# Performance work log

Hardware: AMD Instinct MI355X
Metric: run time of the kernel (lower is better)

The kernel has to match this reference:

```python
import jax, jax.numpy as jnp
import numpy as np


def _conv1x1(x, W, b):
    # x: (B,C,H,W), W: (O,C), b: (O,)
    return jnp.einsum('bchw,oc->bohw', x, W) + b[None, :, None, None]


def _maxpool2(x):
    B, C, H, W = x.shape
    return x.reshape(B, C, H // 2, 2, W // 2, 2).max(axis=(3, 5))


def setup_inputs() -> dict:
    key = jax.random.key(0)
    ks = jax.random.split(key, 6)
    B, C, H, W = 8, 1024, 64, 64
    DI, DO = 512, 1024
    std = 0.01  # matches nn.init.normal_(std=0.01)
    return {
        'x': jax.random.normal(ks[0], (B, C, H, W), dtype=jnp.float32),
        'W_theta': std * jax.random.normal(ks[1], (DI, C), dtype=jnp.float32),
        'b_theta': jnp.zeros((DI,), jnp.float32),
        'W_phi': std * jax.random.normal(ks[2], (DI, C), dtype=jnp.float32),
        'b_phi': jnp.zeros((DI,), jnp.float32),
        'W_g': std * jax.random.normal(ks[3], (DI, C), dtype=jnp.float32),
        'b_g': jnp.zeros((DI,), jnp.float32),
        'W_out': std * jax.random.normal(ks[4], (DO, DI), dtype=jnp.float32),
        'b_out': jnp.zeros((DO,), jnp.float32),
    }


def reference(x, W_theta, b_theta, W_phi, b_phi, W_g, b_g, W_out, b_out):
    B, C, H, W = x.shape
    di = W_theta.shape[0]
    scale = di ** (-0.5)
    # queries from full-res map: (B, di, N) with N = H*W
    theta = _conv1x1(x, W_theta, b_theta).reshape(B, di, H * W)
    # keys/values from 2x2-maxpooled map: (B, di, M), M = (H/2)*(W/2)
    px = _maxpool2(x)
    phi = _conv1x1(px, W_phi, b_phi).reshape(B, di, -1)
    g = _conv1x1(px, W_g, b_g).reshape(B, di, -1)
    # attention: (B, N, M)
    logits = jnp.einsum('bdn,bdm->bnm', theta, phi) * scale
    p = jax.nn.softmax(logits, axis=-1)
    # aggregate values: (B, di, N) -> (B, di, H, W)
    t = jnp.einsum('bdm,bnm->bdn', g, p).reshape(B, di, H, W)
    y = _conv1x1(t, W_out, b_out)
    return y + x
```

## Files before the change

### kernel.cpp

```cpp
#include <hip/hip_runtime.h>
#include <hip/hip_bf16.h>
#include <stdint.h>

typedef __bf16 bf16;
typedef __bf16 bf16x8 __attribute__((ext_vector_type(8)));
typedef __bf16 bf16x4 __attribute__((ext_vector_type(4)));
typedef float f32x4 __attribute__((ext_vector_type(4)));

#define GLOAD_LDS16(gptr, lptr)                                                        \
  __builtin_amdgcn_global_load_lds((const __attribute__((address_space(1))) void*)(gptr), \
                                   (__attribute__((address_space(3))) void*)(lptr), 16, 0, 0)

__global__ __launch_bounds__(256) void cast_f2b(const float* __restrict__ in,
                                                bf16* __restrict__ out, int n) {
  int i = (blockIdx.x * 256 + threadIdx.x) * 4;
  if (i >= n) return;
  const float4 v = *(const float4*)(in + i);
  bf16x4 o;
  o[0] = (bf16)v.x; o[1] = (bf16)v.y; o[2] = (bf16)v.z; o[3] = (bf16)v.w;
  *(bf16x4*)(out + i) = o;
}

__global__ __launch_bounds__(256) void zero_k(float* __restrict__ p, int n) {
  int i = blockIdx.x * 256 + threadIdx.x;
  if (i < n) p[i] = 0.f;
}

__global__ __launch_bounds__(256) void prep_kernel(const float* __restrict__ x,
                                                   bf16* __restrict__ xbT,
                                                   bf16* __restrict__ pxT) {
  const int b = blockIdx.y;
  x   += (size_t)b * 1024 * 4096;
  xbT += (size_t)b * 4096 * 1024;
  pxT += (size_t)b * 1024 * 1024;
  const int bid = blockIdx.x;
  const int h0 = bid & 31, ct = bid >> 5;
  const int tid = threadIdx.x;
  __shared__ float tile[64][129];
  const float* xs = x + (size_t)(ct * 64) * 4096 + h0 * 128;
#pragma unroll
  for (int e = 0; e < 8; ++e) {
    const int idx = e * 256 + tid;
    const int c = idx >> 5, n4 = (idx & 31) * 4;
    *(float4*)&tile[c][n4] = *(const float4*)&xs[(size_t)c * 4096 + n4];
  }
  __syncthreads();
  bf16* xo = xbT + (size_t)(h0 * 128) * 1024 + ct * 64;
#pragma unroll
  for (int e = 0; e < 4; ++e) {
    const int flat = e * 256 + tid;
    const int n = flat >> 3, c8 = (flat & 7) * 8;
    bf16x8 o;
#pragma unroll
    for (int j = 0; j < 8; ++j) o[j] = (bf16)tile[c8 + j][n];
    *(bf16x8*)&xo[(size_t)n * 1024 + c8] = o;
  }
  bf16* po = pxT + (size_t)(h0 * 32) * 1024 + ct * 64;
  {
    const int m = tid >> 3, c8 = (tid & 7) * 8;
    bf16x8 o;
#pragma unroll
    for (int j = 0; j < 8; ++j) {
      const int c = c8 + j;
      float v = fmaxf(fmaxf(tile[c][2 * m], tile[c][2 * m + 1]),
                      fmaxf(tile[c][64 + 2 * m], tile[c][64 + 2 * m + 1]));
      o[j] = (bf16)v;
    }
    *(bf16x8*)&po[(size_t)m * 1024 + c8] = o;
  }
}

template <int EPI>
__global__ __launch_bounds__(512, 4) void gemm256(
    const bf16* __restrict__ A, long long sA, int lda,
    const bf16* __restrict__ B, long long sB, int ldb,
    void* __restrict__ Cv, long long sC, int ldc, int K,
    const float* __restrict__ bias,
    const float* __restrict__ resid, long long sResid, float scale,
    float* __restrict__ rs_out) {
  const int z = blockIdx.z;
  A += (size_t)z * sA;
  B += (size_t)z * sB;
  const int tid = threadIdx.x;
  const int w = tid >> 6, lane = tid & 63;
  const int r16 = lane & 15, q4 = lane >> 4;
  const int wm = w >> 2, wn = w & 3;
  const long long tileM = (long long)blockIdx.x * 128;
  const long long tileN = (long long)blockIdx.y * 256;

  __shared__ bf16 As[2][4096];
  __shared__ bf16 Bs[2][8192];

  f32x4 acc[4][4] = {};

  const int srow = tid >> 2;
  const int skb  = (tid & 3) ^ ((srow >> 1) & 3);
  const char* Ag = (const char*)A + ((size_t)(tileM + srow) * lda + skb * 8) * 2;
  const char* Bg = (const char*)B + ((size_t)(tileN + srow) * ldb + skb * 8) * 2;
  const size_t b128 = (size_t)128 * ldb * 2;

  auto stage = [&](int T) {
    const int sl = T & 1;
    GLOAD_LDS16(Ag + (size_t)T * 64, &As[sl][w * 512]);
    GLOAD_LDS16(Bg + (size_t)T * 64, &Bs[sl][w * 512]);
    GLOAD_LDS16(Bg + (size_t)T * 64 + b128, &Bs[sl][4096 + w * 512]);
  };

  stage(0);
  const int NT = K >> 5;

  for (int T = 0; T < NT; ++T) {
    asm volatile("s_waitcnt vmcnt(0)" ::: "memory");
    __builtin_amdgcn_s_barrier();
    asm volatile("" ::: "memory");
    if (T + 1 < NT) stage(T + 1);
    const char* Asl = (const char*)&As[T & 1][0];
    const char* Bsl = (const char*)&Bs[T & 1][0];
    bf16x8 af[4], bf_[4];
#pragma unroll
    for (int mi = 0; mi < 4; ++mi) {
      const int row = wm * 64 + mi * 16 + r16;
      af[mi] = *(const bf16x8*)(Asl + row * 64 + ((q4 ^ ((row >> 1) & 3)) << 4));
    }
#pragma unroll
    for (int ni = 0; ni < 4; ++ni) {
      const int row = wn * 64 + ni * 16 + r16;
      bf_[ni] = *(const bf16x8*)(Bsl + row * 64 + ((q4 ^ ((row >> 1) & 3)) << 4));
    }
    __builtin_amdgcn_s_setprio(1);
#pragma unroll
    for (int mi = 0; mi < 4; ++mi)
#pragma unroll
      for (int ni = 0; ni < 4; ++ni)
        acc[mi][ni] = __builtin_amdgcn_mfma_f32_16x16x32_bf16(af[mi], bf_[ni], acc[mi][ni], 0, 0, 0);
    __builtin_amdgcn_s_setprio(0);
  }

  if constexpr (EPI == 4) {
    float* C = (float*)Cv + (size_t)z * sC;
    const float* rz = resid + (size_t)z * sResid;
#pragma unroll
    for (int a = 0; a < 4; ++a) {
      const int row0 = (int)tileM + wm * 64 + a * 16 + q4 * 4;
#pragma unroll
      for (int ni = 0; ni < 4; ++ni) {
        const int col = (int)tileN + wn * 64 + ni * 16 + r16;
#pragma unroll
        for (int r = 0; r < 4; ++r)
          C[(size_t)(row0 + r) * ldc + col] =
              acc[a][ni][r] + bias[row0 + r] + rz[(size_t)(row0 + r) * ldc + col];
      }
    }
  } else if constexpr (EPI == 5) {
    bf16* C = (bf16*)Cv + (size_t)z * sC;
    float* rsp = rs_out + (size_t)z * 4096;
#pragma unroll
    for (int a = 0; a < 4; ++a) {
      const int row0 = (int)tileM + wm * 64 + a * 16 + q4 * 4;
      float psum[4] = {0.f, 0.f, 0.f, 0.f};
#pragma unroll
      for (int ni = 0; ni < 4; ++ni) {
        const int col = (int)tileN + wn * 64 + ni * 16 + r16;
#pragma unroll
        for (int r = 0; r < 4; ++r) {
          float e = __expf(acc[a][ni][r]);
          psum[r] += e;
          C[(size_t)(row0 + r) * ldc + col] = (bf16)e;
        }
      }
#pragma unroll
      for (int r = 0; r < 4; ++r) {
        float v = psum[r];
        v += __shfl_xor(v, 1);
        v += __shfl_xor(v, 2);
        v += __shfl_xor(v, 4);
        v += __shfl_xor(v, 8);
        if (r16 == 0) atomicAdd(&rsp[row0 + r], v);
      }
    }
  } else if constexpr (EPI == 7) {
    bf16* C = (bf16*)Cv + (size_t)z * sC;
    const float* rsp = bias + (size_t)z * 4096;
#pragma unroll
    for (int a = 0; a < 4; ++a) {
      const int row0 = (int)tileM + wm * 64 + a * 16 + q4 * 4;
      float inv[4];
#pragma unroll
      for (int r = 0; r < 4; ++r) inv[r] = 1.0f / rsp[row0 + r];
#pragma unroll
      for (int ni = 0; ni < 4; ++ni) {
        const int col = (int)tileN + wn * 64 + ni * 16 + r16;
#pragma unroll
        for (int r = 0; r < 4; ++r)
          C[(size_t)(row0 + r) * ldc + col] = (bf16)(acc[a][ni][r] * inv[r]);
      }
    }
  } else if constexpr (EPI == 2) {
    bf16* C = (bf16*)Cv + (size_t)z * sC;
#pragma unroll
    for (int a = 0; a < 4; ++a) {
      const int row0 = (int)tileM + wm * 64 + a * 16 + q4 * 4;
#pragma unroll
      for (int ni = 0; ni < 4; ++ni) {
        const int col = (int)tileN + wn * 64 + ni * 16 + r16;
#pragma unroll
        for (int r = 0; r < 4; ++r)
          C[(size_t)(row0 + r) * ldc + col] = (bf16)(acc[a][ni][r] + bias[row0 + r]);
      }
    }
  } else {
    bf16* C = (bf16*)Cv + (size_t)z * sC;
#pragma unroll
    for (int a = 0; a < 4; ++a) {
      const int row0 = (int)tileM + wm * 64 + a * 16 + q4 * 4;
#pragma unroll
      for (int ni = 0; ni < 4; ++ni) {
        const int col = (int)tileN + wn * 64 + ni * 16 + r16;
        const float badd = bias[col];
#pragma unroll
        for (int r = 0; r < 4; ++r)
          C[(size_t)(row0 + r) * ldc + col] = (bf16)((acc[a][ni][r] + badd) * scale);
      }
    }
  }
}

extern "C" void kernel_launch(void* const* d_in, const int* in_sizes, int n_in,
                              void* d_out, int out_size, void* d_ws, size_t ws_size,
                              hipStream_t stream) {
  const float* x  = (const float*)d_in[0];
  const float* Wt = (const float*)d_in[1];
  const float* bt = (const float*)d_in[2];
  const float* Wp = (const float*)d_in[3];
  const float* bp = (const float*)d_in[4];
  const float* Wg = (const float*)d_in[5];
  const float* bg = (const float*)d_in[6];
  const float* Wo = (const float*)d_in[7];
  const float* bo = (const float*)d_in[8];
  float* out = (float*)d_out;

  const size_t MB = 1024ull * 1024ull;
  char* ws = (char*)d_ws;
  bf16* WtB = (bf16*)(ws + 0 * MB);
  bf16* WpB = (bf16*)(ws + 1 * MB);
  bf16* WgB = (bf16*)(ws + 2 * MB);
  bf16* WoB = (bf16*)(ws + 3 * MB);

  cast_f2b<<<512, 256, 0, stream>>>(Wt, WtB, 512 * 1024);
  cast_f2b<<<512, 256, 0, stream>>>(Wp, WpB, 512 * 1024);
  cast_f2b<<<512, 256, 0, stream>>>(Wg, WgB, 512 * 1024);
  cast_f2b<<<512, 256, 0, stream>>>(Wo, WoB, 1024 * 512);

  const float SCALE = 0.044194173824159216f;

  auto run_g6 = [&](int nb, int b0, bf16* tT) {
    gemm256<4><<<dim3(8, 16, nb), 512, 0, stream>>>(WoB, 0, 512, tT, 4096ll * 512, 512,
                                                    out + (size_t)b0 * 1024 * 4096,
                                                    1024ll * 4096, 4096, 512,
                                                    bo, x + (size_t)b0 * 1024 * 4096,
                                                    1024ll * 4096, 1.f, nullptr);
  };

  if (ws_size >= 164 * MB) {
    bf16* pxT    = (bf16*)(ws + 4 * MB);
    bf16* phiT   = (bf16*)(ws + 20 * MB);
    bf16* g      = (bf16*)(ws + 28 * MB);
    bf16* thetaT = (bf16*)(ws + 36 * MB);
    bf16* tT     = (bf16*)(ws + 68 * MB);
    bf16* xbT    = (bf16*)(ws + 100 * MB);
    bf16*  Pt   = (bf16*)d_out;
    float* rsum = (float*)((char*)d_out + 80 * MB);

    prep_kernel<<<dim3(512, 8), 256, 0, stream>>>(x, xbT, pxT);
    gemm256<1><<<dim3(32, 2, 8), 512, 0, stream>>>(xbT, 4096ll * 1024, 1024, WtB, 0, 1024,
                                                   thetaT, 4096ll * 512, 512, 1024,
                                                   bt, nullptr, 0, SCALE, nullptr);
    gemm256<1><<<dim3(8, 2, 8), 512, 0, stream>>>(pxT, 1024ll * 1024, 1024, WpB, 0, 1024,
                                                  phiT, 1024ll * 512, 512, 1024,
                                                  bp, nullptr, 0, 1.f, nullptr);
    gemm256<2><<<dim3(4, 4, 8), 512, 0, stream>>>(WgB, 0, 1024, pxT, 1024ll * 1024, 1024,
                                                  g, 512ll * 1024, 1024, 1024,
                                                  bg, nullptr, 0, 1.f, nullptr);
    zero_k<<<128, 256, 0, stream>>>(rsum, 32768);
    gemm256<5><<<dim3(32, 4, 8), 512, 0, stream>>>(thetaT, 4096ll * 512, 512,
                                                   phiT, 1024ll * 512, 512,
                                                   Pt, 4096ll * 1024, 1024, 512,
                                                   nullptr, nullptr, 0, 1.f, rsum);
    gemm256<7><<<dim3(32, 2, 8), 512, 0, stream>>>(Pt, 4096ll * 1024, 1024,
                                                   g, 512ll * 1024, 1024,
                                                   tT, 4096ll * 512, 512, 1024,
                                                   rsum, nullptr, 0, 1.f, nullptr);
    run_g6(8, 0, tT);
  } else if (ws_size >= 108 * MB) {
    bf16* pxT    = (bf16*)(ws + 4 * MB);
    bf16* phiT   = (bf16*)(ws + 20 * MB);
    bf16* g      = (bf16*)(ws + 28 * MB);
    bf16* thetaT = (bf16*)(ws + 36 * MB);
    bf16* tT     = (bf16*)(ws + 68 * MB);
    bf16* xbT    = (bf16*)(ws + 100 * MB);
    float* rsum = (float*)((char*)d_out + 80 * MB);
    for (int b = 0; b < 8; ++b) {
      prep_kernel<<<dim3(512, 1), 256, 0, stream>>>(x + (size_t)b * 1024 * 4096, xbT,
                                                    pxT + (size_t)b * 1024 * 1024);
      gemm256<1><<<dim3(32, 2, 1), 512, 0, stream>>>(xbT, 0, 1024, WtB, 0, 1024,
                                                     thetaT + (size_t)b * 4096 * 512, 0, 512,
                                                     1024, bt, nullptr, 0, SCALE, nullptr);
    }
    gemm256<1><<<dim3(8, 2, 8), 512, 0, stream>>>(pxT, 1024ll * 1024, 1024, WpB, 0, 1024,
                                                  phiT, 1024ll * 512, 512, 1024,
                                                  bp, nullptr, 0, 1.f, nullptr);
    gemm256<2><<<dim3(4, 4, 8), 512, 0, stream>>>(WgB, 0, 1024, pxT, 1024ll * 1024, 1024,
                                                  g, 512ll * 1024, 1024, 1024,
                                                  bg, nullptr, 0, 1.f, nullptr);
    for (int b = 0; b < 8; ++b) {
      bf16* Ptb = (bf16*)d_out + (size_t)b * 4096 * 1024;
      zero_k<<<16, 256, 0, stream>>>(rsum + (size_t)b * 4096, 4096);
      gemm256<5><<<dim3(32, 4, 1), 512, 0, stream>>>(thetaT + (size_t)b * 4096 * 512, 0, 512,
                                                     phiT + (size_t)b * 1024 * 512, 0, 512,
                                                     Ptb, 0, 1024, 512,
                                                     nullptr, nullptr, 0, 1.f,
                                                     rsum + (size_t)b * 4096);
      gemm256<7><<<dim3(32, 2, 1), 512, 0, stream>>>(Ptb, 0, 1024,
                                                     g + (size_t)b * 512 * 1024, 0, 1024,
                                                     tT + (size_t)b * 4096 * 512, 0, 512, 1024,
                                                     rsum + (size_t)b * 4096, nullptr, 0, 1.f,
                                                     nullptr);
    }
    run_g6(8, 0, tT);
  } else {
    float* rsum  = (float*)(ws + 4 * MB);
    bf16* pxT    = (bf16*)(ws + 5 * MB);
    bf16* phiT   = (bf16*)(ws + 7 * MB);
    bf16* g      = (bf16*)(ws + 8 * MB);
    bf16* thetaT = (bf16*)(ws + 9 * MB);
    bf16* tT     = (bf16*)(ws + 13 * MB);
    bf16* Pt     = (bf16*)(ws + 17 * MB);
    bf16* xbT    = (bf16*)(ws + 25 * MB);
    for (int b = 0; b < 8; ++b) {
      prep_kernel<<<dim3(512, 1), 256, 0, stream>>>(x + (size_t)b * 1024 * 4096, xbT, pxT);
      gemm256<1><<<dim3(32, 2, 1), 512, 0, stream>>>(xbT, 0, 1024, WtB, 0, 1024,
                                                     thetaT, 0, 512, 1024,
                                                     bt, nullptr, 0, SCALE, nullptr);
      gemm256<1><<<dim3(8, 2, 1), 512, 0, stream>>>(pxT, 0, 1024, WpB, 0, 1024,
                                                    phiT, 0, 512, 1024,
                                                    bp, nullptr, 0, 1.f, nullptr);
      gemm256<2><<<dim3(4, 4, 1), 512, 0, stream>>>(WgB, 0, 1024, pxT, 0, 1024,
                                                    g, 0, 1024, 1024,
                                                    bg, nullptr, 0, 1.f, nullptr);
      zero_k<<<16, 256, 0, stream>>>(rsum, 4096);
      gemm256<5><<<dim3(32, 4, 1), 512, 0, stream>>>(thetaT, 0, 512, phiT, 0, 512,
                                                     Pt, 0, 1024, 512,
                                                     nullptr, nullptr, 0, 1.f, rsum);
      gemm256<7><<<dim3(32, 2, 1), 512, 0, stream>>>(Pt, 0, 1024, g, 0, 1024,
                                                     tT, 0, 512, 1024,
                                                     rsum, nullptr, 0, 1.f, nullptr);
      run_g6(1, b, tT);
    }
  }
}
```

Measured before the change: 323.4 us.

## Reassociate output projection with values and fuse phi/g projections

Precomputes W2 = W_out·g per batch so the final GEMM multiplies W2 by the unnormalized attention matrix directly, dropping the separate P·g GEMM and the tT intermediate. The softmax normalization, bias and residual are applied in a new epilogue. The phi and g projections are merged into one GEMM with concatenated weights and biases. In exchange, the final GEMM's reduction length doubles, and a new W2 GEMM is added.

```diff
diff --git a/kernel.cpp b/kernel.cpp
--- a/kernel.cpp
+++ b/kernel.cpp
@@ -24,6 +24,14 @@
 __global__ __launch_bounds__(256) void zero_k(float* __restrict__ p, int n) {
   int i = blockIdx.x * 256 + threadIdx.x;
   if (i < n) p[i] = 0.f;
+}
+
+__global__ __launch_bounds__(256) void concat512(const float* __restrict__ a,
+                                                 const float* __restrict__ b,
+                                                 float* __restrict__ o) {
+  int i = blockIdx.x * 256 + threadIdx.x;
+  if (i < 512) o[i] = a[i];
+  else if (i < 1024) o[i] = b[i - 512];
 }
 
 __global__ __launch_bounds__(256) void prep_kernel(const float* __restrict__ x,
@@ -114,6 +122,7 @@
     __builtin_amdgcn_s_barrier();
     asm volatile("" ::: "memory");
     if (T + 1 < NT) stage(T + 1);
+
     const char* Asl = (const char*)&As[T & 1][0];
     const char* Bsl = (const char*)&Bs[T & 1][0];
     bf16x8 af[4], bf_[4];
@@ -149,6 +158,26 @@
         for (int r = 0; r < 4; ++r)
           C[(size_t)(row0 + r) * ldc + col] =
               acc[a][ni][r] + bias[row0 + r] + rz[(size_t)(row0 + r) * ldc + col];
+      }
+    }
+  } else if constexpr (EPI == 8) {
+    float* C = (float*)Cv + (size_t)z * sC;
+    const float* rz = resid + (size_t)z * sResid;
+    const float* rsp = rs_out + (size_t)z * 4096;
+#pragma unroll
+    for (int a = 0; a < 4; ++a) {
+      const int row0 = (int)tileM + wm * 64 + a * 16 + q4 * 4;
+      float bv[4];
+#pragma unroll
+      for (int r = 0; r < 4; ++r) bv[r] = bias[row0 + r];
+#pragma unroll
+      for (int ni = 0; ni < 4; ++ni) {
+        const int col = (int)tileN + wn * 64 + ni * 16 + r16;
+        const float cinv = 1.0f / rsp[col];
+#pragma unroll
+        for (int r = 0; r < 4; ++r)
+          C[(size_t)(row0 + r) * ldc + col] =
+              acc[a][ni][r] * cinv + bv[r] + rz[(size_t)(row0 + r) * ldc + col];
       }
     }
   } else if constexpr (EPI == 5) {
@@ -206,6 +235,19 @@
 #pragma unroll
         for (int r = 0; r < 4; ++r)
           C[(size_t)(row0 + r) * ldc + col] = (bf16)(acc[a][ni][r] + bias[row0 + r]);
+      }
+    }
+  } else if constexpr (EPI == 0) {
+    bf16* C = (bf16*)Cv + (size_t)z * sC;
+#pragma unroll
+    for (int a = 0; a < 4; ++a) {
+      const int row0 = (int)tileM + wm * 64 + a * 16 + q4 * 4;
+#pragma unroll
+      for (int ni = 0; ni < 4; ++ni) {
+        const int col = (int)tileN + wn * 64 + ni * 16 + r16;
+#pragma unroll
+        for (int r = 0; r < 4; ++r)
+          C[(size_t)(row0 + r) * ldc + col] = (bf16)acc[a][ni][r];
       }
     }
   } else {
@@ -241,57 +283,50 @@
 
   const size_t MB = 1024ull * 1024ull;
   char* ws = (char*)d_ws;
-  bf16* WtB = (bf16*)(ws + 0 * MB);
-  bf16* WpB = (bf16*)(ws + 1 * MB);
-  bf16* WgB = (bf16*)(ws + 2 * MB);
-  bf16* WoB = (bf16*)(ws + 3 * MB);
+  bf16* WtB  = (bf16*)(ws + 0 * MB);
+  bf16* WoB  = (bf16*)(ws + 1 * MB);
+  bf16* WpgB = (bf16*)(ws + 2 * MB);
 
   cast_f2b<<<512, 256, 0, stream>>>(Wt, WtB, 512 * 1024);
-  cast_f2b<<<512, 256, 0, stream>>>(Wp, WpB, 512 * 1024);
-  cast_f2b<<<512, 256, 0, stream>>>(Wg, WgB, 512 * 1024);
   cast_f2b<<<512, 256, 0, stream>>>(Wo, WoB, 1024 * 512);
+  cast_f2b<<<512, 256, 0, stream>>>(Wp, WpgB, 512 * 1024);
+  cast_f2b<<<512, 256, 0, stream>>>(Wg, WpgB + 512 * 1024, 512 * 1024);
 
   const float SCALE = 0.044194173824159216f;
 
-  auto run_g6 = [&](int nb, int b0, bf16* tT) {
-    gemm256<4><<<dim3(8, 16, nb), 512, 0, stream>>>(WoB, 0, 512, tT, 4096ll * 512, 512,
-                                                    out + (size_t)b0 * 1024 * 4096,
-                                                    1024ll * 4096, 4096, 512,
-                                                    bo, x + (size_t)b0 * 1024 * 4096,
-                                                    1024ll * 4096, 1.f, nullptr);
-  };
-
   if (ws_size >= 164 * MB) {
-    bf16* pxT    = (bf16*)(ws + 4 * MB);
-    bf16* phiT   = (bf16*)(ws + 20 * MB);
-    bf16* g      = (bf16*)(ws + 28 * MB);
-    bf16* thetaT = (bf16*)(ws + 36 * MB);
-    bf16* tT     = (bf16*)(ws + 68 * MB);
+    float* bias_pg = (float*)(ws + 4 * MB);
+    float* rsum    = (float*)(ws + 4 * MB + 65536);
+    bf16* pxT    = (bf16*)(ws + 5 * MB);
+    bf16* pg     = (bf16*)(ws + 21 * MB);
+    bf16* thetaT = (bf16*)(ws + 37 * MB);
+    bf16* W2     = (bf16*)(ws + 69 * MB);
     bf16* xbT    = (bf16*)(ws + 100 * MB);
-    bf16*  Pt   = (bf16*)d_out;
-    float* rsum = (float*)((char*)d_out + 80 * MB);
-
+    bf16* Pt     = xbT;
+
+    concat512<<<4, 256, 0, stream>>>(bp, bg, bias_pg);
     prep_kernel<<<dim3(512, 8), 256, 0, stream>>>(x, xbT, pxT);
     gemm256<1><<<dim3(32, 2, 8), 512, 0, stream>>>(xbT, 4096ll * 1024, 1024, WtB, 0, 1024,
                                                    thetaT, 4096ll * 512, 512, 1024,
                                                    bt, nullptr, 0, SCALE, nullptr);
-    gemm256<1><<<dim3(8, 2, 8), 512, 0, stream>>>(pxT, 1024ll * 1024, 1024, WpB, 0, 1024,
-                                                  phiT, 1024ll * 512, 512, 1024,
-                                                  bp, nullptr, 0, 1.f, nullptr);
-    gemm256<2><<<dim3(4, 4, 8), 512, 0, stream>>>(WgB, 0, 1024, pxT, 1024ll * 1024, 1024,
-                                                  g, 512ll * 1024, 1024, 1024,
-                                                  bg, nullptr, 0, 1.f, nullptr);
+    gemm256<1><<<dim3(8, 4, 8), 512, 0, stream>>>(pxT, 1024ll * 1024, 1024, WpgB, 0, 1024,
+                                                  pg, 1024ll * 1024, 1024, 1024,
+                                                  bias_pg, nullptr, 0, 1.f, nullptr);
+    gemm256<0><<<dim3(8, 4, 8), 512, 0, stream>>>(WoB, 0, 512, pg + 512, 1024ll * 1024, 1024,
+                                                  W2, 1024ll * 1024, 1024, 512,
+                                                  nullptr, nullptr, 0, 1.f, nullptr);
     zero_k<<<128, 256, 0, stream>>>(rsum, 32768);
     gemm256<5><<<dim3(32, 4, 8), 512, 0, stream>>>(thetaT, 4096ll * 512, 512,
-                                                   phiT, 1024ll * 512, 512,
+                                                   pg, 1024ll * 1024, 1024,
                                                    Pt, 4096ll * 1024, 1024, 512,
                                                    nullptr, nullptr, 0, 1.f, rsum);
-    gemm256<7><<<dim3(32, 2, 8), 512, 0, stream>>>(Pt, 4096ll * 1024, 1024,
-                                                   g, 512ll * 1024, 1024,
-                                                   tT, 4096ll * 512, 512, 1024,
-                                                   rsum, nullptr, 0, 1.f, nullptr);
-    run_g6(8, 0, tT);
+    gemm256<8><<<dim3(8, 16, 8), 512, 0, stream>>>(W2, 1024ll * 1024, 1024,
+                                                   Pt, 4096ll * 1024, 1024,
+                                                   out, 1024ll * 4096, 4096, 1024,
+                                                   bo, x, 1024ll * 4096, 1.f, rsum);
   } else if (ws_size >= 108 * MB) {
+    bf16* WpB = WpgB;
+    bf16* WgB = WpgB + 512 * 1024;
     bf16* pxT    = (bf16*)(ws + 4 * MB);
     bf16* phiT   = (bf16*)(ws + 20 * MB);
     bf16* g      = (bf16*)(ws + 28 * MB);
@@ -326,8 +361,12 @@
                                                      rsum + (size_t)b * 4096, nullptr, 0, 1.f,
                                                      nullptr);
     }
-    run_g6(8, 0, tT);
+    gemm256<4><<<dim3(8, 16, 8), 512, 0, stream>>>(WoB, 0, 512, tT, 4096ll * 512, 512,
+                                                   out, 1024ll * 4096, 4096, 512,
+                                                   bo, x, 1024ll * 4096, 1.f, nullptr);
   } else {
+    bf16* WpB = WpgB;
+    bf16* WgB = WpgB + 512 * 1024;
     float* rsum  = (float*)(ws + 4 * MB);
     bf16* pxT    = (bf16*)(ws + 5 * MB);
     bf16* phiT   = (bf16*)(ws + 7 * MB);
@@ -354,7 +393,11 @@
       gemm256<7><<<dim3(32, 2, 1), 512, 0, stream>>>(Pt, 0, 1024, g, 0, 1024,
                                                      tT, 0, 512, 1024,
                                                      rsum, nullptr, 0, 1.f, nullptr);
-      run_g6(1, b, tT);
-    }
-  }
-}
+      gemm256<4><<<dim3(8, 16, 1), 512, 0, stream>>>(WoB, 0, 512, tT, 0, 512,
+                                                     out + (size_t)b * 1024 * 4096,
+                                                     1024ll * 4096, 4096, 512,
+                                                     bo, x + (size_t)b * 1024 * 4096,
+                                                     1024ll * 4096, 1.f, nullptr);
+    }
+  }
+}
```

After: 320.9 us. No clear change (-0.8%).
